# Performance work log

Measured on AMD Instinct MI355X. Metric: run time of the kernel, lower is better.

## Reference

```python
import jax, jax.numpy as jnp
import numpy as np

B, WIN = 2048, 11          # batch, hardcoded window_size=11
K, VOCAB = 4096, 30522     # hash dim, bert-base-uncased vocab
NOUT, TOPK = 18, 64        # action logits, top-k active hash bits
THRESH = 1e-10


def setup_inputs() -> dict:
    key = jax.random.key(0)
    k1, k2, k3 = jax.random.split(key, 3)
    # avoid id 0 (padding) so sentence_lengths > 0
    ids = jax.random.randint(k1, (B, 1, WIN), 1, VOCAB, dtype=jnp.int32)
    W = jax.random.normal(k2, (K, VOCAB, 2), dtype=jnp.float32)  # view_as_complex layout
    w_out = jax.random.normal(k3, (NOUT, K), dtype=jnp.float32) * 0.02
    b_out = jnp.zeros((NOUT,), dtype=jnp.float32)
    return {"ids": ids, "W": W, "w_out": w_out, "b_out": b_out}


def reference(ids, W, w_out, b_out):
    ids2 = ids.reshape(ids.shape[0], ids.shape[-1])
    nz = (ids2 != 0)
    position_ids = jnp.cumsum(nz, axis=-1)
    sl = nz.sum(-1)
    sl = jnp.where(sl > 0, sl, ids2.shape[-1])                   # fallback branch
    pos = jnp.pi * position_ids / sl[:, None].astype(jnp.float32)
    o_re, o_im = jnp.cos(pos), jnp.sin(pos)

    Wre, Wim = W[..., 0], W[..., 1]                              # complex W parts [K, V]
    g_re = jnp.take(Wre, ids2, axis=1)
    g_im = jnp.take(Wim, ids2, axis=1)
    W_abs = jnp.sqrt(g_re * g_re + g_im * g_im)

    # phis = W_indices * conj(one_roots): (a+bi)(c-di)
    p_re = g_re * o_re + g_im * o_im
    p_im = g_im * o_re - g_re * o_im
    # clamp tiny real/imag components to +THRESH (matches torch r_phis edit)
    p_re = jnp.where((p_re < THRESH) & (p_re > -THRESH), THRESH, p_re)
    p_im = jnp.where((p_im < THRESH) & (p_im > -THRESH), THRESH, p_im)
    ang = jnp.abs(jnp.arctan2(p_im, p_re))

    phi_factor = (W_abs + ang) * nz                              # added_factors=True
    pf = phi_factor.sum(-1).T                                    # [B, K]

    # argsort descending, take top k, scatter True -> binary hash
    _, idx = jax.lax.top_k(pf, TOPK)                             # [B, TOPK]
    rows = jnp.arange(pf.shape[0])[:, None]
    feat = jnp.zeros_like(pf).at[rows, idx].set(1.0)             # [B, K] float

    logits = feat @ w_out.T + b_out                              # [B, NOUT]
    return logits
```

## Files before the change

kernel.cpp:

```cpp
#include <hip/hip_runtime.h>
#include <hip/hip_bf16.h>
#include <stdint.h>

#define B_     2048
#define WIN_   11
#define K_     4096
#define VOCAB_ 30522
#define NOUT_  18
#define TOPK_  64
#define NPAIR_ (B_ * WIN_)
#define PI_F   3.14159274101257324f

#define NCH_    15
#define CHUNK_  2048
#define UNITS_  1024
#define UPK_    15261
#define TAILU_  925
#define KPB_    16
#define NBLK_   (K_ / KPB_)
#define GTOT_   (NCH_ * KPB_)
#define PFTH_   1024
#define PRT_    256
#define CNT_    768
#define PCON_BYTES_ (NPAIR_ * 4)
#define SMEM_BYTES_ (PCON_BYTES_ + 4 * CHUNK_ * 8)

static_assert(GTOT_ % 4 == 0, "unroll-4 rotation");

typedef float vf4 __attribute__((ext_vector_type(4)));

__global__ void prep_kernel(const int* __restrict__ ids, int* __restrict__ tabv) {
    int b = blockIdx.x * blockDim.x + threadIdx.x;
    if (b >= B_) return;
    const int* row = ids + b * WIN_;
    int poss[WIN_];
    int cnt = 0;
#pragma unroll
    for (int w = 0; w < WIN_; ++w) { cnt += (row[w] != 0); poss[w] = cnt; }
    int sl = (cnt > 0) ? cnt : WIN_;
#pragma unroll
    for (int w = 0; w < WIN_; ++w) {
        int tb = (poss[w] - 1) * 11 + (sl - 1);
        if (tb < 0) tb = 0;
        tabv[b * WIN_ + w] = tb;
    }
}

__global__ __launch_bounds__(512) void bucket_kernel(const int* __restrict__ ids,
                                                     const int* __restrict__ tabv,
                                                     int2* __restrict__ smeta,
                                                     int* __restrict__ chunkstart) {
    __shared__ int lcnt[512 * NCH_];
    __shared__ int segtot[NCH_][8];
    __shared__ int tot[NCH_];
    __shared__ int bbase[NCH_ + 1];
    const int t = threadIdx.x;

#pragma unroll
    for (int c = 0; c < NCH_; ++c) lcnt[t * NCH_ + c] = 0;
    __syncthreads();

    for (int p = t; p < NPAIR_; p += 512) {
        int id = ids[p];
        if (id != 0) lcnt[t * NCH_ + (id / CHUNK_)] += 1;
    }
    __syncthreads();

    if (t < NCH_ * 8) {
        int bkt = t >> 3, seg = t & 7;
        int run = 0;
        for (int i = 0; i < 64; ++i) {
            int idx = (seg * 64 + i) * NCH_ + bkt;
            int tmp = lcnt[idx];
            lcnt[idx] = run;
            run += tmp;
        }
        segtot[bkt][seg] = run;
    }
    __syncthreads();
    if (t < NCH_) {
        int run = 0;
#pragma unroll
        for (int s = 0; s < 8; ++s) { int tmp = segtot[t][s]; segtot[t][s] = run; run += tmp; }
        tot[t] = run;
    }
    __syncthreads();
    if (t == 0) {
        int run = 0;
#pragma unroll
        for (int c = 0; c < NCH_; ++c) { bbase[c] = run; run += tot[c]; }
        bbase[NCH_] = run;
#pragma unroll
        for (int c = 0; c <= NCH_; ++c) chunkstart[c] = bbase[c];
    }
    __syncthreads();
    if (t < NCH_ * 8) {
        int bkt = t >> 3, seg = t & 7;
        int add = segtot[bkt][seg];
        for (int i = 0; i < 64; ++i) lcnt[(seg * 64 + i) * NCH_ + bkt] += add;
    }
    __syncthreads();

    for (int p = t; p < NPAIR_; p += 512) {
        int id = ids[p];
        if (id == 0) continue;
        int bkt = id / CHUNK_;
        int pos = bbase[bkt] + lcnt[t * NCH_ + bkt];
        lcnt[t * NCH_ + bkt] += 1;
        int2 mm;
        mm.x = id;
        mm.y = p | (tabv[p] << 16);
        smeta[pos] = mm;
    }
}

__device__ __forceinline__ void pair_body2(const int2 m, const float2* __restrict__ sb,
                                           int lo, const float2* __restrict__ trig,
                                           float* __restrict__ pcontrib) {
    int id  = m.x;
    int dst = m.y & 0xFFFF;
    int tab = m.y >> 16;
    float2 o = trig[tab];
    float2 g = sb[id - lo];
    float wabs = sqrtf(__fadd_rn(__fmul_rn(g.x, g.x), __fmul_rn(g.y, g.y)));
    float pre = __fadd_rn(__fmul_rn(g.x, o.x), __fmul_rn(g.y, o.y));
    float pim = __fsub_rn(__fmul_rn(g.y, o.x), __fmul_rn(g.x, o.y));
    if (pre < 1e-10f && pre > -1e-10f) pre = 1e-10f;
    if (pim < 1e-10f && pim > -1e-10f) pim = 1e-10f;
    float ang = fabsf(atan2f(pim, pre));
    pcontrib[dst] = __fadd_rn(wabs, ang);
}

__global__ __launch_bounds__(PFTH_, 1) void pf_kernel(const vf4* __restrict__ W4,
                                                      const int2* __restrict__ smeta,
                                                      const int* __restrict__ chunkstart,
                                                      float* __restrict__ pfT) {
    extern __shared__ char smem[];
    float* pcontrib = (float*)smem;
    char*  sbuf     = smem + PCON_BYTES_;
    __shared__ int cstart[NCH_ + 1];
    __shared__ float2 trigS[121];

    const int t = threadIdx.x;
    const int kbase = blockIdx.x * KPB_;

    if (t <= NCH_) cstart[t] = chunkstart[t];
    if (t < 121) {
        int pp = t / 11 + 1, ss = t % 11 + 1;
        float pos = __fdiv_rn(__fmul_rn(PI_F, (float)pp), (float)ss);
        trigS[t] = make_float2(cosf(pos), sinf(pos));
    }

#define LOADCH(GP, R0, R1, R2, R3)                                               \
    {   int g2_ = (GP);                                                          \
        if (g2_ < GTOT_) {                                                       \
            int kk2_ = g2_ / NCH_, cc2_ = g2_ % NCH_;                            \
            int nu2_ = (cc2_ == NCH_ - 1) ? TAILU_ : UNITS_;                     \
            const vf4* s2_ = W4 + (size_t)(kbase + kk2_) * UPK_ + (size_t)cc2_ * UNITS_; \
            if (t < nu2_)            R0 = __builtin_nontemporal_load(&s2_[t]);   \
            if (PRT_ + t < nu2_)     R1 = __builtin_nontemporal_load(&s2_[PRT_ + t]); \
            if (2 * PRT_ + t < nu2_) R2 = __builtin_nontemporal_load(&s2_[2 * PRT_ + t]); \
            if (3 * PRT_ + t < nu2_) R3 = __builtin_nontemporal_load(&s2_[3 * PRT_ + t]); \
        }                                                                        \
    }

    vf4 a0, a1, a2, a3, b0, b1, b2, b3, c0, c1, c2, c3, d0, d1, d2, d3;
    int2 A0{}, A1{}, B0{}, B1{};

    if (t < PRT_) {
        LOADCH(0, a0, a1, a2, a3)
        {   vf4* db = (vf4*)sbuf;
            db[t] = a0; db[PRT_ + t] = a1;
            db[2 * PRT_ + t] = a2; db[3 * PRT_ + t] = a3; }
        LOADCH(1, b0, b1, b2, b3)
        LOADCH(2, c0, c1, c2, c3)
        LOADCH(3, d0, d1, d2, d3)
    } else {
        int ct = t - PRT_;
        int q0 = ct;         if (q0 > NPAIR_ - 1) q0 = NPAIR_ - 1;
        int q1 = CNT_ + ct;  if (q1 > NPAIR_ - 1) q1 = NPAIR_ - 1;
        A0 = smeta[q0]; A1 = smeta[q1];
    }
    for (int i = t; i < NPAIR_; i += PFTH_) pcontrib[i] = 0.0f;
    asm volatile("s_waitcnt vmcnt(0) lgkmcnt(0)" ::: "memory");
    __builtin_amdgcn_s_barrier();
    __builtin_amdgcn_sched_barrier(0);

#define PHASE(J, L0, L1, L2, L3, Wr0, Wr1, Wr2, Wr3, SU0, SU1, SL0, SL1)         \
    {                                                                            \
        const int p_ = g + (J);                                                  \
        __builtin_amdgcn_sched_barrier(0);                                       \
        asm volatile("s_waitcnt lgkmcnt(0)" ::: "memory");                       \
        __builtin_amdgcn_s_barrier();                                            \
        __builtin_amdgcn_sched_barrier(0);                                       \
        int ccj_ = cc + (J); int kkj_ = kk;                                      \
        if (ccj_ >= NCH_) { ccj_ -= NCH_; kkj_ += 1; }                           \
        if (t < PRT_) {                                                          \
            if (p_ + 1 < GTOT_) {                                                \
                int cw_ = ccj_ + 1; if (cw_ >= NCH_) cw_ = 0;                    \
                int nw_ = (cw_ == NCH_ - 1) ? TAILU_ : UNITS_;                   \
                vf4* db_ = (vf4*)(sbuf + (size_t)((p_ + 1) & 3) * (CHUNK_ * 8)); \
                if (t < nw_)            db_[t] = Wr0;                            \
                if (PRT_ + t < nw_)     db_[PRT_ + t] = Wr1;                     \
                if (2 * PRT_ + t < nw_) db_[2 * PRT_ + t] = Wr2;                 \
                if (3 * PRT_ + t < nw_) db_[3 * PRT_ + t] = Wr3;                 \
            }                                                                    \
            LOADCH(p_ + 4, L0, L1, L2, L3)                                       \
        } else {                                                                 \
            const int ct_ = t - PRT_;                                            \
            {   int cn_ = ccj_ + 1; if (cn_ >= NCH_) cn_ = 0;                    \
                int ns_ = cstart[cn_];                                           \
                int q0_ = ns_ + ct_;         if (q0_ > NPAIR_ - 1) q0_ = NPAIR_ - 1; \
                int q1_ = ns_ + CNT_ + ct_;  if (q1_ > NPAIR_ - 1) q1_ = NPAIR_ - 1; \
                SL0 = smeta[q0_]; SL1 = smeta[q1_]; }                            \
            {   const float2* sb_ = (const float2*)(sbuf + (size_t)(p_ & 3) * (CHUNK_ * 8)); \
                const int lo_ = ccj_ * CHUNK_;                                   \
                const int cs_ = cstart[ccj_], ce_ = cstart[ccj_ + 1];            \
                if (cs_ + ct_ < ce_)        pair_body2(SU0, sb_, lo_, trigS, pcontrib); \
                if (cs_ + CNT_ + ct_ < ce_) pair_body2(SU1, sb_, lo_, trigS, pcontrib); \
                for (int pp_ = cs_ + 2 * CNT_ + ct_; pp_ < ce_; pp_ += CNT_)     \
                    pair_body2(smeta[pp_], sb_, lo_, trigS, pcontrib); }         \
        }                                                                        \
        if (ccj_ == NCH_ - 1) {                                                  \
            __builtin_amdgcn_sched_barrier(0);                                   \
            asm volatile("s_waitcnt lgkmcnt(0)" ::: "memory");                   \
            __builtin_amdgcn_s_barrier();                                        \
            __builtin_amdgcn_sched_barrier(0);                                   \
            float* outp_ = pfT + (size_t)(kbase + kkj_) * B_;                    \
            _Pragma("unroll")                                                    \
            for (int i_ = 0; i_ < B_ / PFTH_; ++i_) {                            \
                int b_ = i_ * PFTH_ + t;                                         \
                float acc_ = 0.0f;                                               \
                _Pragma("unroll")                                                \
                for (int w_ = 0; w_ < WIN_; ++w_)                                \
                    acc_ = __fadd_rn(acc_, pcontrib[b_ * WIN_ + w_]);            \
                outp_[b_] = acc_;                                                \
            }                                                                    \
        }                                                                        \
    }

#pragma unroll 1
    for (int g = 0; g < GTOT_; g += 4) {
        const int cc = g % NCH_, kk = g / NCH_;
        PHASE(0, a0, a1, a2, a3, b0, b1, b2, b3, A0, A1, B0, B1)
        PHASE(1, b0, b1, b2, b3, c0, c1, c2, c3, B0, B1, A0, A1)
        PHASE(2, c0, c1, c2, c3, d0, d1, d2, d3, A0, A1, B0, B1)
        PHASE(3, d0, d1, d2, d3, a0, a1, a2, a3, B0, B1, A0, A1)
    }
#undef PHASE
#undef LOADCH
}

__global__ __launch_bounds__(256) void transpose_kb(const float* __restrict__ pfT,
                                                    float* __restrict__ pf) {
    __shared__ float tile[64][65];
    int kb = blockIdx.x * 64;
    int bb = blockIdx.y * 64;
    int tx = threadIdx.x & 63;
    int ty = threadIdx.x >> 6;
#pragma unroll
    for (int i = 0; i < 64; i += 4)
        tile[ty + i][tx] = pfT[(size_t)(kb + ty + i) * B_ + (bb + tx)];
    __syncthreads();
#pragma unroll
    for (int i = 0; i < 64; i += 4)
        pf[(size_t)(bb + ty + i) * K_ + (kb + tx)] = tile[tx][ty + i];
}

__global__ __launch_bounds__(256) void topk_logits_kernel(const float* __restrict__ pf,
                                                          const float* __restrict__ w_out,
                                                          const float* __restrict__ b_out,
                                                          float* __restrict__ out) {
    const int b = blockIdx.x;
    const int t = threadIdx.x;
    __shared__ uint32_t srow[K_];
    __shared__ int hist[256];
    __shared__ int sfx[256];
    __shared__ uint32_t sh_prefix;
    __shared__ int sh_need;
    __shared__ int wave_gt[4], wave_eq[4];
    __shared__ int gt_running, eq_running;
    __shared__ int idxlist[TOPK_];
    __shared__ float partial[4][NOUT_];

    const float* rowp = pf + (size_t)b * K_;
    for (int i = t; i < K_; i += 256) srow[i] = __float_as_uint(rowp[i]);
    if (t == 0) { sh_prefix = 0u; sh_need = TOPK_; gt_running = 0; eq_running = 0; }
    __syncthreads();

    for (int pass = 0; pass < 4; ++pass) {
        int shift = 24 - 8 * pass;
        uint32_t himask = (pass == 0) ? 0u : (0xFFFFFFFFu << (shift + 8));
        hist[t] = 0;
        __syncthreads();
        uint32_t prefix = sh_prefix & himask;
        for (int i = t; i < K_; i += 256) {
            uint32_t u = srow[i];
            if ((u & himask) == prefix) atomicAdd(&hist[(u >> shift) & 255], 1);
        }
        __syncthreads();
        sfx[t] = hist[t];
        __syncthreads();
#pragma unroll
        for (int off = 1; off < 256; off <<= 1) {
            int v = (t + off < 256) ? sfx[t + off] : 0;
            __syncthreads();
            sfx[t] += v;
            __syncthreads();
        }
        int need = sh_need;
        int above = (t == 255) ? 0 : sfx[t + 1];
        if (sfx[t] >= need && above < need) {
            sh_prefix |= ((uint32_t)t << shift);
            sh_need = need - above;
        }
        __syncthreads();
    }
    const uint32_t T = sh_prefix;
    const int r = sh_need;
    const int c_gt = TOPK_ - r;

    for (int cbase = 0; cbase < K_; cbase += 256) {
        uint32_t u = srow[cbase + t];
        bool gt = (u > T);
        bool eq = (u == T);
        unsigned long long mg = __ballot(gt);
        unsigned long long me = __ballot(eq);
        int lane = t & 63, wv = t >> 6;
        if (lane == 0) { wave_gt[wv] = __popcll(mg); wave_eq[wv] = __popcll(me); }
        __syncthreads();
        int offg = gt_running, offe = eq_running;
        for (int w2 = 0; w2 < wv; ++w2) { offg += wave_gt[w2]; offe += wave_eq[w2]; }
        unsigned long long lmask = (lane == 0) ? 0ull : ((~0ull) >> (64 - lane));
        int rkg = offg + __popcll(mg & lmask);
        int rke = offe + __popcll(me & lmask);
        if (gt) idxlist[rkg] = cbase + t;
        else if (eq && rke < r) idxlist[c_gt + rke] = cbase + t;
        __syncthreads();
        if (t == 0) {
            gt_running += wave_gt[0] + wave_gt[1] + wave_gt[2] + wave_gt[3];
            eq_running += wave_eq[0] + wave_eq[1] + wave_eq[2] + wave_eq[3];
        }
        __syncthreads();
    }

    {
        int lane = t & 63, wv4 = t >> 6;
        if (lane < NOUT_) {
            const float* wrow = w_out + (size_t)lane * K_;
            float s = 0.0f;
#pragma unroll
            for (int j = 0; j < TOPK_ / 4; ++j) s += wrow[idxlist[wv4 * (TOPK_ / 4) + j]];
            partial[wv4][lane] = s;
        }
        __syncthreads();
        if (t < NOUT_) {
            float s = b_out[t] + partial[0][t] + partial[1][t] + partial[2][t] + partial[3][t];
            out[b * NOUT_ + t] = s;
        }
    }
}

extern "C" void kernel_launch(void* const* d_in, const int* in_sizes, int n_in,
                              void* d_out, int out_size, void* d_ws, size_t ws_size,
                              hipStream_t stream) {
    const int*   ids   = (const int*)d_in[0];
    const float* W     = (const float*)d_in[1];
    const float* w_out = (const float*)d_in[2];
    const float* b_out = (const float*)d_in[3];
    float* out = (float*)d_out;

    char* ws = (char*)d_ws;
    const size_t pf_bytes = (size_t)K_ * B_ * sizeof(float);
    float* pfT   = (float*)(ws);
    float* pf    = (float*)(ws + pf_bytes);
    int*   tabv  = (int*)(ws + 2 * pf_bytes);
    int2*  smeta = (int2*)(ws + 2 * pf_bytes + 256 * 1024);
    int* chunkstart = (int*)(ws + 2 * pf_bytes + 768 * 1024);

    (void)hipFuncSetAttribute((const void*)pf_kernel,
                              hipFuncAttributeMaxDynamicSharedMemorySize,
                              SMEM_BYTES_);

    prep_kernel<<<(B_ + 255) / 256, 256, 0, stream>>>(ids, tabv);
    bucket_kernel<<<1, 512, 0, stream>>>(ids, tabv, smeta, chunkstart);
    pf_kernel<<<NBLK_, PFTH_, SMEM_BYTES_, stream>>>((const vf4*)W, smeta, chunkstart, pfT);
    transpose_kb<<<dim3(K_ / 64, B_ / 64), 256, 0, stream>>>(pfT, pf);
    topk_logits_kernel<<<B_, 256, 0, stream>>>(pf, w_out, b_out, out);
}
```

Measured before the change: 404.5 us.

## Process two vocab chunks per barrier window with 16 smaller chunks

Re-splits each K-row of W into 16 chunks of 954 vec4 units instead of 15 of 1024, so chunk and k indices come from shifts and masks rather than division. Each barrier window now streams and computes two chunks, which halves the number of block-wide barriers and lets the loader and compute threads issue twice as much work per sync. Register use rises from doubled load registers and six prefetched metadata pairs per thread, which may lower occupancy. The ring still has four LDS buffers, so reuse ordering between loads, writes and compute needs care.

```diff
diff --git a/kernel.cpp b/kernel.cpp
--- a/kernel.cpp
+++ b/kernel.cpp
@@ -11,21 +11,23 @@
 #define NPAIR_ (B_ * WIN_)
 #define PI_F   3.14159274101257324f
 
-#define NCH_    15
-#define CHUNK_  2048
-#define UNITS_  1024
+#define NCH_    16
+#define CHUNK_  1908
+#define CUNITS_ 954
+#define TAILU_  951
 #define UPK_    15261
-#define TAILU_  925
+#define BUFB_   (CHUNK_ * 8)
 #define KPB_    16
 #define NBLK_   (K_ / KPB_)
 #define GTOT_   (NCH_ * KPB_)
+#define NWIN_   (GTOT_ / 2)
 #define PFTH_   1024
 #define PRT_    256
 #define CNT_    768
 #define PCON_BYTES_ (NPAIR_ * 4)
-#define SMEM_BYTES_ (PCON_BYTES_ + 4 * CHUNK_ * 8)
-
-static_assert(GTOT_ % 4 == 0, "unroll-4 rotation");
+#define SMEM_BYTES_ (PCON_BYTES_ + 4 * BUFB_)
+
+static_assert(NWIN_ % 2 == 0, "window ping-pong");
 
 typedef float vf4 __attribute__((ext_vector_type(4)));
 
@@ -150,104 +152,122 @@
         float pos = __fdiv_rn(__fmul_rn(PI_F, (float)pp), (float)ss);
         trigS[t] = make_float2(cosf(pos), sinf(pos));
     }
-
-#define LOADCH(GP, R0, R1, R2, R3)                                               \
-    {   int g2_ = (GP);                                                          \
+    __syncthreads();
+
+#define LOADCH(G, R0, R1, R2, R3)                                                \
+    {   int g2_ = (G);                                                           \
         if (g2_ < GTOT_) {                                                       \
-            int kk2_ = g2_ / NCH_, cc2_ = g2_ % NCH_;                            \
-            int nu2_ = (cc2_ == NCH_ - 1) ? TAILU_ : UNITS_;                     \
-            const vf4* s2_ = W4 + (size_t)(kbase + kk2_) * UPK_ + (size_t)cc2_ * UNITS_; \
-            if (t < nu2_)            R0 = __builtin_nontemporal_load(&s2_[t]);   \
-            if (PRT_ + t < nu2_)     R1 = __builtin_nontemporal_load(&s2_[PRT_ + t]); \
-            if (2 * PRT_ + t < nu2_) R2 = __builtin_nontemporal_load(&s2_[2 * PRT_ + t]); \
-            if (3 * PRT_ + t < nu2_) R3 = __builtin_nontemporal_load(&s2_[3 * PRT_ + t]); \
+            int kk2_ = g2_ >> 4, cc2_ = g2_ & 15;                                \
+            int nu2_ = (cc2_ == 15) ? TAILU_ : CUNITS_;                          \
+            const vf4* s2_ = W4 + (size_t)(kbase + kk2_) * UPK_ + (size_t)cc2_ * CUNITS_; \
+            R0 = __builtin_nontemporal_load(&s2_[t]);                            \
+            R1 = __builtin_nontemporal_load(&s2_[256 + t]);                      \
+            R2 = __builtin_nontemporal_load(&s2_[512 + t]);                      \
+            if (768 + t < nu2_) R3 = __builtin_nontemporal_load(&s2_[768 + t]);  \
         }                                                                        \
     }
 
-    vf4 a0, a1, a2, a3, b0, b1, b2, b3, c0, c1, c2, c3, d0, d1, d2, d3;
-    int2 A0{}, A1{}, B0{}, B1{};
+#define WRITECH(G, R0, R1, R2, R3)                                               \
+    {   int g2_ = (G);                                                           \
+        if (g2_ < GTOT_) {                                                       \
+            int cc2_ = g2_ & 15;                                                 \
+            int nu2_ = (cc2_ == 15) ? TAILU_ : CUNITS_;                          \
+            vf4* db_ = (vf4*)(sbuf + (size_t)(g2_ & 3) * BUFB_);                 \
+            db_[t] = R0; db_[256 + t] = R1; db_[512 + t] = R2;                   \
+            if (768 + t < nu2_) db_[768 + t] = R3;                               \
+        }                                                                        \
+    }
+
+#define SMLOAD(G, M0, M1, M2)                                                    \
+    {   int cc2_ = (G) & 15;                                                     \
+        int ns_ = cstart[cc2_];                                                  \
+        int q0_ = ns_ + ct;            if (q0_ > NPAIR_ - 1) q0_ = NPAIR_ - 1;   \
+        int q1_ = ns_ + CNT_ + ct;     if (q1_ > NPAIR_ - 1) q1_ = NPAIR_ - 1;   \
+        int q2_ = ns_ + 2 * CNT_ + ct; if (q2_ > NPAIR_ - 1) q2_ = NPAIR_ - 1;   \
+        M0 = smeta[q0_]; M1 = smeta[q1_]; M2 = smeta[q2_]; }
+
+#define SMCOMP(G, M0, M1, M2)                                                    \
+    {   int cc2_ = (G) & 15;                                                     \
+        const float2* sb_ = (const float2*)(sbuf + (size_t)((G) & 3) * BUFB_);   \
+        const int lo_ = cc2_ * CHUNK_;                                           \
+        const int cs_ = cstart[cc2_], ce_ = cstart[cc2_ + 1];                    \
+        if (cs_ + ct < ce_)           pair_body2(M0, sb_, lo_, trigS, pcontrib); \
+        if (cs_ + CNT_ + ct < ce_)    pair_body2(M1, sb_, lo_, trigS, pcontrib); \
+        if (cs_ + 2 * CNT_ + ct < ce_) pair_body2(M2, sb_, lo_, trigS, pcontrib);\
+        for (int pp_ = cs_ + 3 * CNT_ + ct; pp_ < ce_; pp_ += CNT_)              \
+            pair_body2(smeta[pp_], sb_, lo_, trigS, pcontrib); }
+
+    vf4 a0, a1, a2, a3, a4, a5, a6, a7;
+    vf4 b0, b1, b2, b3, b4, b5, b6, b7;
+    int2 mA0{}, mA1{}, mA2{}, mA3{}, mA4{}, mA5{};
+    int2 mB0{}, mB1{}, mB2{}, mB3{}, mB4{}, mB5{};
+    const int ct = (t >= PRT_) ? (t - PRT_) : 0;
 
     if (t < PRT_) {
         LOADCH(0, a0, a1, a2, a3)
-        {   vf4* db = (vf4*)sbuf;
-            db[t] = a0; db[PRT_ + t] = a1;
-            db[2 * PRT_ + t] = a2; db[3 * PRT_ + t] = a3; }
-        LOADCH(1, b0, b1, b2, b3)
-        LOADCH(2, c0, c1, c2, c3)
-        LOADCH(3, d0, d1, d2, d3)
+        LOADCH(1, a4, a5, a6, a7)
+        WRITECH(0, a0, a1, a2, a3)
+        WRITECH(1, a4, a5, a6, a7)
+        LOADCH(2, b0, b1, b2, b3)
+        LOADCH(3, b4, b5, b6, b7)
     } else {
-        int ct = t - PRT_;
-        int q0 = ct;         if (q0 > NPAIR_ - 1) q0 = NPAIR_ - 1;
-        int q1 = CNT_ + ct;  if (q1 > NPAIR_ - 1) q1 = NPAIR_ - 1;
-        A0 = smeta[q0]; A1 = smeta[q1];
+        SMLOAD(0, mA0, mA1, mA2)
+        SMLOAD(1, mA3, mA4, mA5)
     }
     for (int i = t; i < NPAIR_; i += PFTH_) pcontrib[i] = 0.0f;
     asm volatile("s_waitcnt vmcnt(0) lgkmcnt(0)" ::: "memory");
     __builtin_amdgcn_s_barrier();
     __builtin_amdgcn_sched_barrier(0);
 
-#define PHASE(J, L0, L1, L2, L3, Wr0, Wr1, Wr2, Wr3, SU0, SU1, SL0, SL1)         \
+#define WINDOW(WJ, L0,L1,L2,L3,L4,L5,L6,L7, S0,S1,S2,S3,S4,S5,S6,S7,            \
+               U0,U1,U2,U3,U4,U5, V0,V1,V2,V3,V4,V5)                             \
     {                                                                            \
-        const int p_ = g + (J);                                                  \
+        const int w_ = (WJ);                                                     \
         __builtin_amdgcn_sched_barrier(0);                                       \
         asm volatile("s_waitcnt lgkmcnt(0)" ::: "memory");                       \
         __builtin_amdgcn_s_barrier();                                            \
         __builtin_amdgcn_sched_barrier(0);                                       \
-        int ccj_ = cc + (J); int kkj_ = kk;                                      \
-        if (ccj_ >= NCH_) { ccj_ -= NCH_; kkj_ += 1; }                           \
         if (t < PRT_) {                                                          \
-            if (p_ + 1 < GTOT_) {                                                \
-                int cw_ = ccj_ + 1; if (cw_ >= NCH_) cw_ = 0;                    \
-                int nw_ = (cw_ == NCH_ - 1) ? TAILU_ : UNITS_;                   \
-                vf4* db_ = (vf4*)(sbuf + (size_t)((p_ + 1) & 3) * (CHUNK_ * 8)); \
-                if (t < nw_)            db_[t] = Wr0;                            \
-                if (PRT_ + t < nw_)     db_[PRT_ + t] = Wr1;                     \
-                if (2 * PRT_ + t < nw_) db_[2 * PRT_ + t] = Wr2;                 \
-                if (3 * PRT_ + t < nw_) db_[3 * PRT_ + t] = Wr3;                 \
-            }                                                                    \
-            LOADCH(p_ + 4, L0, L1, L2, L3)                                       \
+            LOADCH(2 * w_ + 4, L0, L1, L2, L3)                                   \
+            LOADCH(2 * w_ + 5, L4, L5, L6, L7)                                   \
+            WRITECH(2 * w_ + 2, S0, S1, S2, S3)                                  \
+            WRITECH(2 * w_ + 3, S4, S5, S6, S7)                                  \
         } else {                                                                 \
-            const int ct_ = t - PRT_;                                            \
-            {   int cn_ = ccj_ + 1; if (cn_ >= NCH_) cn_ = 0;                    \
-                int ns_ = cstart[cn_];                                           \
-                int q0_ = ns_ + ct_;         if (q0_ > NPAIR_ - 1) q0_ = NPAIR_ - 1; \
-                int q1_ = ns_ + CNT_ + ct_;  if (q1_ > NPAIR_ - 1) q1_ = NPAIR_ - 1; \
-                SL0 = smeta[q0_]; SL1 = smeta[q1_]; }                            \
-            {   const float2* sb_ = (const float2*)(sbuf + (size_t)(p_ & 3) * (CHUNK_ * 8)); \
-                const int lo_ = ccj_ * CHUNK_;                                   \
-                const int cs_ = cstart[ccj_], ce_ = cstart[ccj_ + 1];            \
-                if (cs_ + ct_ < ce_)        pair_body2(SU0, sb_, lo_, trigS, pcontrib); \
-                if (cs_ + CNT_ + ct_ < ce_) pair_body2(SU1, sb_, lo_, trigS, pcontrib); \
-                for (int pp_ = cs_ + 2 * CNT_ + ct_; pp_ < ce_; pp_ += CNT_)     \
-                    pair_body2(smeta[pp_], sb_, lo_, trigS, pcontrib); }         \
+            SMLOAD(2 * w_ + 2, V0, V1, V2)                                       \
+            SMLOAD(2 * w_ + 3, V3, V4, V5)                                       \
+            SMCOMP(2 * w_,     U0, U1, U2)                                       \
+            SMCOMP(2 * w_ + 1, U3, U4, U5)                                       \
         }                                                                        \
-        if (ccj_ == NCH_ - 1) {                                                  \
+        if (((2 * w_ + 1) & 15) == 15) {                                         \
             __builtin_amdgcn_sched_barrier(0);                                   \
-            asm volatile("s_waitcnt lgkmcnt(0)" ::: "memory");                   \
+            asm volatile("s_waitcnt lgkmcnt(0)" ::: "memory");                    \
             __builtin_amdgcn_s_barrier();                                        \
             __builtin_amdgcn_sched_barrier(0);                                   \
-            float* outp_ = pfT + (size_t)(kbase + kkj_) * B_;                    \
+            const int kk_ = (2 * w_) >> 4;                                       \
+            float* outp_ = pfT + (size_t)(kbase + kk_) * B_;                     \
             _Pragma("unroll")                                                    \
             for (int i_ = 0; i_ < B_ / PFTH_; ++i_) {                            \
-                int b_ = i_ * PFTH_ + t;                                         \
+                int bb_ = i_ * PFTH_ + t;                                        \
                 float acc_ = 0.0f;                                               \
                 _Pragma("unroll")                                                \
-                for (int w_ = 0; w_ < WIN_; ++w_)                                \
-                    acc_ = __fadd_rn(acc_, pcontrib[b_ * WIN_ + w_]);            \
-                outp_[b_] = acc_;                                                \
+                for (int ww_ = 0; ww_ < WIN_; ++ww_)                             \
+                    acc_ = __fadd_rn(acc_, pcontrib[bb_ * WIN_ + ww_]);          \
+                outp_[bb_] = acc_;                                               \
             }                                                                    \
         }                                                                        \
     }
 
 #pragma unroll 1
-    for (int g = 0; g < GTOT_; g += 4) {
-        const int cc = g % NCH_, kk = g / NCH_;
-        PHASE(0, a0, a1, a2, a3, b0, b1, b2, b3, A0, A1, B0, B1)
-        PHASE(1, b0, b1, b2, b3, c0, c1, c2, c3, B0, B1, A0, A1)
-        PHASE(2, c0, c1, c2, c3, d0, d1, d2, d3, A0, A1, B0, B1)
-        PHASE(3, d0, d1, d2, d3, a0, a1, a2, a3, B0, B1, A0, A1)
-    }
-#undef PHASE
+    for (int w = 0; w < NWIN_; w += 2) {
+        WINDOW(w,     a0,a1,a2,a3,a4,a5,a6,a7, b0,b1,b2,b3,b4,b5,b6,b7,
+               mA0,mA1,mA2,mA3,mA4,mA5, mB0,mB1,mB2,mB3,mB4,mB5)
+        WINDOW(w + 1, b0,b1,b2,b3,b4,b5,b6,b7, a0,a1,a2,a3,a4,a5,a6,a7,
+               mB0,mB1,mB2,mB3,mB4,mB5, mA0,mA1,mA2,mA3,mA4,mA5)
+    }
+#undef WINDOW
+#undef SMCOMP
+#undef SMLOAD
+#undef WRITECH
 #undef LOADCH
 }
 
```

Measured after the change: 550.5 us. +36.1%, slower.

## Stream W chunks via direct global-to-LDS loads and shrink producer wave group

Applied to the files above, without the earlier changes.

Replaces the register-staged W chunk pipeline (global load into VGPRs, then ds_write) with global_load_lds async copies into a 4-deep LDS ring, gated by vmcnt waits. The producer group drops from 256 to 64 threads, so 960 threads now do the pair compute and the final reduction. This is meant to remove the VGPR round trip and spread the compute over more lanes, at the cost of more in-flight loads per producer thread. It also depends on getting the vmcnt accounting and buffer indexing right.

```diff
diff --git a/kernel.cpp b/kernel.cpp
--- a/kernel.cpp
+++ b/kernel.cpp
@@ -14,20 +14,17 @@
 #define NCH_    15
 #define CHUNK_  2048
 #define UNITS_  1024
-#define UPK_    15261
 #define TAILU_  925
 #define KPB_    16
 #define NBLK_   (K_ / KPB_)
 #define GTOT_   (NCH_ * KPB_)
 #define PFTH_   1024
-#define PRT_    256
-#define CNT_    768
+#define PRT_    64
+#define CNT_    960
 #define PCON_BYTES_ (NPAIR_ * 4)
 #define SMEM_BYTES_ (PCON_BYTES_ + 4 * CHUNK_ * 8)
 
-static_assert(GTOT_ % 4 == 0, "unroll-4 rotation");
-
-typedef float vf4 __attribute__((ext_vector_type(4)));
+static_assert(GTOT_ % 2 == 0, "2-phase ping-pong");
 
 __global__ void prep_kernel(const int* __restrict__ ids, int* __restrict__ tabv) {
     int b = blockIdx.x * blockDim.x + threadIdx.x;
@@ -131,7 +128,7 @@
     pcontrib[dst] = __fadd_rn(wabs, ang);
 }
 
-__global__ __launch_bounds__(PFTH_, 1) void pf_kernel(const vf4* __restrict__ W4,
+__global__ __launch_bounds__(PFTH_, 1) void pf_kernel(const float* __restrict__ W,
                                                       const int2* __restrict__ smeta,
                                                       const int* __restrict__ chunkstart,
                                                       float* __restrict__ pfT) {
@@ -145,110 +142,98 @@
     const int kbase = blockIdx.x * KPB_;
 
     if (t <= NCH_) cstart[t] = chunkstart[t];
-    if (t < 121) {
-        int pp = t / 11 + 1, ss = t % 11 + 1;
+    if (t >= 128 && t < 128 + 121) {
+        int i = t - 128;
+        int pp = i / 11 + 1, ss = i % 11 + 1;
         float pos = __fdiv_rn(__fmul_rn(PI_F, (float)pp), (float)ss);
-        trigS[t] = make_float2(cosf(pos), sinf(pos));
-    }
-
-#define LOADCH(GP, R0, R1, R2, R3)                                               \
-    {   int g2_ = (GP);                                                          \
-        if (g2_ < GTOT_) {                                                       \
-            int kk2_ = g2_ / NCH_, cc2_ = g2_ % NCH_;                            \
-            int nu2_ = (cc2_ == NCH_ - 1) ? TAILU_ : UNITS_;                     \
-            const vf4* s2_ = W4 + (size_t)(kbase + kk2_) * UPK_ + (size_t)cc2_ * UNITS_; \
-            if (t < nu2_)            R0 = __builtin_nontemporal_load(&s2_[t]);   \
-            if (PRT_ + t < nu2_)     R1 = __builtin_nontemporal_load(&s2_[PRT_ + t]); \
-            if (2 * PRT_ + t < nu2_) R2 = __builtin_nontemporal_load(&s2_[2 * PRT_ + t]); \
-            if (3 * PRT_ + t < nu2_) R3 = __builtin_nontemporal_load(&s2_[3 * PRT_ + t]); \
-        }                                                                        \
-    }
-
-    vf4 a0, a1, a2, a3, b0, b1, b2, b3, c0, c1, c2, c3, d0, d1, d2, d3;
+        trigS[i] = make_float2(cosf(pos), sinf(pos));
+    }
+    __syncthreads();
+
+    auto stage = [&](int cl, int kl, int buf) {
+        const int n16 = (cl == NCH_ - 1) ? TAILU_ : UNITS_;
+        const char* gb = (const char*)W +
+            ((size_t)(kbase + kl) * VOCAB_ + (size_t)cl * CHUNK_) * 8;
+        char* lb = sbuf + (size_t)buf * (CHUNK_ * 8);
+#pragma unroll
+        for (int j = 0; j < 16; ++j) {
+            int u = j * 64 + t;
+            int uc = (u < n16) ? u : (n16 - 1);
+            __builtin_amdgcn_global_load_lds(
+                (const __attribute__((address_space(1))) void*)(gb + (size_t)uc * 16),
+                (__attribute__((address_space(3))) void*)(lb + (size_t)j * 1024),
+                16, 0, 0);
+        }
+    };
+
     int2 A0{}, A1{}, B0{}, B1{};
+    const int ct = (t >= PRT_) ? (t - PRT_) : 0;
 
     if (t < PRT_) {
-        LOADCH(0, a0, a1, a2, a3)
-        {   vf4* db = (vf4*)sbuf;
-            db[t] = a0; db[PRT_ + t] = a1;
-            db[2 * PRT_ + t] = a2; db[3 * PRT_ + t] = a3; }
-        LOADCH(1, b0, b1, b2, b3)
-        LOADCH(2, c0, c1, c2, c3)
-        LOADCH(3, d0, d1, d2, d3)
+        stage(0, 0, 0);
+        stage(1, 0, 1);
+        stage(2, 0, 2);
     } else {
-        int ct = t - PRT_;
         int q0 = ct;         if (q0 > NPAIR_ - 1) q0 = NPAIR_ - 1;
         int q1 = CNT_ + ct;  if (q1 > NPAIR_ - 1) q1 = NPAIR_ - 1;
         A0 = smeta[q0]; A1 = smeta[q1];
     }
     for (int i = t; i < NPAIR_; i += PFTH_) pcontrib[i] = 0.0f;
-    asm volatile("s_waitcnt vmcnt(0) lgkmcnt(0)" ::: "memory");
-    __builtin_amdgcn_s_barrier();
-    __builtin_amdgcn_sched_barrier(0);
-
-#define PHASE(J, L0, L1, L2, L3, Wr0, Wr1, Wr2, Wr3, SU0, SU1, SL0, SL1)         \
+
+    int cc = 0, kk = 0;
+
+#define PHASE(GG, CU0, CU1, NX0, NX1)                                            \
     {                                                                            \
-        const int p_ = g + (J);                                                  \
         __builtin_amdgcn_sched_barrier(0);                                       \
         asm volatile("s_waitcnt lgkmcnt(0)" ::: "memory");                       \
+        if (t < PRT_) { asm volatile("s_waitcnt vmcnt(32)" ::: "memory"); }      \
         __builtin_amdgcn_s_barrier();                                            \
         __builtin_amdgcn_sched_barrier(0);                                       \
-        int ccj_ = cc + (J); int kkj_ = kk;                                      \
-        if (ccj_ >= NCH_) { ccj_ -= NCH_; kkj_ += 1; }                           \
         if (t < PRT_) {                                                          \
-            if (p_ + 1 < GTOT_) {                                                \
-                int cw_ = ccj_ + 1; if (cw_ >= NCH_) cw_ = 0;                    \
-                int nw_ = (cw_ == NCH_ - 1) ? TAILU_ : UNITS_;                   \
-                vf4* db_ = (vf4*)(sbuf + (size_t)((p_ + 1) & 3) * (CHUNK_ * 8)); \
-                if (t < nw_)            db_[t] = Wr0;                            \
-                if (PRT_ + t < nw_)     db_[PRT_ + t] = Wr1;                     \
-                if (2 * PRT_ + t < nw_) db_[2 * PRT_ + t] = Wr2;                 \
-                if (3 * PRT_ + t < nw_) db_[3 * PRT_ + t] = Wr3;                 \
-            }                                                                    \
-            LOADCH(p_ + 4, L0, L1, L2, L3)                                       \
+            int cl = cc + 3, kl = kk;                                            \
+            if (cl >= NCH_) { cl -= NCH_; kl += 1; }                             \
+            if ((GG) + 3 >= GTOT_) { cl = NCH_ - 1; kl = KPB_ - 1; }             \
+            stage(cl, kl, ((GG) + 3) & 3);                                       \
         } else {                                                                 \
-            const int ct_ = t - PRT_;                                            \
-            {   int cn_ = ccj_ + 1; if (cn_ >= NCH_) cn_ = 0;                    \
-                int ns_ = cstart[cn_];                                           \
-                int q0_ = ns_ + ct_;         if (q0_ > NPAIR_ - 1) q0_ = NPAIR_ - 1; \
-                int q1_ = ns_ + CNT_ + ct_;  if (q1_ > NPAIR_ - 1) q1_ = NPAIR_ - 1; \
-                SL0 = smeta[q0_]; SL1 = smeta[q1_]; }                            \
-            {   const float2* sb_ = (const float2*)(sbuf + (size_t)(p_ & 3) * (CHUNK_ * 8)); \
-                const int lo_ = ccj_ * CHUNK_;                                   \
-                const int cs_ = cstart[ccj_], ce_ = cstart[ccj_ + 1];            \
-                if (cs_ + ct_ < ce_)        pair_body2(SU0, sb_, lo_, trigS, pcontrib); \
-                if (cs_ + CNT_ + ct_ < ce_) pair_body2(SU1, sb_, lo_, trigS, pcontrib); \
-                for (int pp_ = cs_ + 2 * CNT_ + ct_; pp_ < ce_; pp_ += CNT_)     \
-                    pair_body2(smeta[pp_], sb_, lo_, trigS, pcontrib); }         \
+            {   int cn = cc + 1; if (cn >= NCH_) cn = 0;                         \
+                int ns = cstart[cn];                                             \
+                int q0 = ns + ct;         if (q0 > NPAIR_ - 1) q0 = NPAIR_ - 1;  \
+                int q1 = ns + CNT_ + ct;  if (q1 > NPAIR_ - 1) q1 = NPAIR_ - 1;  \
+                NX0 = smeta[q0]; NX1 = smeta[q1]; }                              \
+            {   const float2* sb = (const float2*)(sbuf + (size_t)((GG) & 3) * (CHUNK_ * 8)); \
+                const int lo = cc * CHUNK_;                                      \
+                const int cs = cstart[cc], ce = cstart[cc + 1];                  \
+                if (cs + ct < ce)         pair_body2(CU0, sb, lo, trigS, pcontrib); \
+                if (cs + CNT_ + ct < ce)  pair_body2(CU1, sb, lo, trigS, pcontrib); \
+                for (int pp = cs + 2 * CNT_ + ct; pp < ce; pp += CNT_)           \
+                    pair_body2(smeta[pp], sb, lo, trigS, pcontrib); }            \
         }                                                                        \
-        if (ccj_ == NCH_ - 1) {                                                  \
+        if (cc == NCH_ - 1) {                                                    \
             __builtin_amdgcn_sched_barrier(0);                                   \
             asm volatile("s_waitcnt lgkmcnt(0)" ::: "memory");                   \
             __builtin_amdgcn_s_barrier();                                        \
             __builtin_amdgcn_sched_barrier(0);                                   \
-            float* outp_ = pfT + (size_t)(kbase + kkj_) * B_;                    \
-            _Pragma("unroll")                                                    \
-            for (int i_ = 0; i_ < B_ / PFTH_; ++i_) {                            \
-                int b_ = i_ * PFTH_ + t;                                         \
-                float acc_ = 0.0f;                                               \
-                _Pragma("unroll")                                                \
-                for (int w_ = 0; w_ < WIN_; ++w_)                                \
-                    acc_ = __fadd_rn(acc_, pcontrib[b_ * WIN_ + w_]);            \
-                outp_[b_] = acc_;                                                \
+            if (t >= PRT_) {                                                     \
+                float* outp = pfT + (size_t)(kbase + kk) * B_;                   \
+                for (int bb = ct; bb < B_; bb += CNT_) {                         \
+                    float acc = 0.0f;                                            \
+                    _Pragma("unroll")                                            \
+                    for (int w = 0; w < WIN_; ++w)                               \
+                        acc = __fadd_rn(acc, pcontrib[bb * WIN_ + w]);           \
+                    outp[bb] = acc;                                              \
+                }                                                                \
             }                                                                    \
-        }                                                                        \
+            cc = 0; ++kk;                                                        \
+        } else { ++cc; }                                                         \
     }
 
 #pragma unroll 1
-    for (int g = 0; g < GTOT_; g += 4) {
-        const int cc = g % NCH_, kk = g / NCH_;
-        PHASE(0, a0, a1, a2, a3, b0, b1, b2, b3, A0, A1, B0, B1)
-        PHASE(1, b0, b1, b2, b3, c0, c1, c2, c3, B0, B1, A0, A1)
-        PHASE(2, c0, c1, c2, c3, d0, d1, d2, d3, A0, A1, B0, B1)
-        PHASE(3, d0, d1, d2, d3, a0, a1, a2, a3, B0, B1, A0, A1)
+    for (int g = 0; g < GTOT_; g += 2) {
+        PHASE(g,     A0, A1, B0, B1)
+        PHASE(g + 1, B0, B1, A0, A1)
     }
 #undef PHASE
-#undef LOADCH
+    asm volatile("s_waitcnt vmcnt(0) lgkmcnt(0)" ::: "memory");
 }
 
 __global__ __launch_bounds__(256) void transpose_kb(const float* __restrict__ pfT,
@@ -384,7 +369,7 @@
 
     prep_kernel<<<(B_ + 255) / 256, 256, 0, stream>>>(ids, tabv);
     bucket_kernel<<<1, 512, 0, stream>>>(ids, tabv, smeta, chunkstart);
-    pf_kernel<<<NBLK_, PFTH_, SMEM_BYTES_, stream>>>((const vf4*)W, smeta, chunkstart, pfT);
+    pf_kernel<<<NBLK_, PFTH_, SMEM_BYTES_, stream>>>(W, smeta, chunkstart, pfT);
     transpose_kb<<<dim3(K_ / 64, B_ / 64), 256, 0, stream>>>(pfT, pf);
     topk_logits_kernel<<<B_, 256, 0, stream>>>(pf, w_out, b_out, out);
 }
```

After: 435.2 us. +7.6%, slower.
